# Kernel optimization log

Hardware: AMD Instinct MI355X
Metric: run time of the kernel (lower is better)

The kernel has to match this reference:

```python
import math
import jax, jax.numpy as jnp
import numpy as np

NUM_OPS = 7
NUM_STAGES = 2
TAU = 1.0


def _stage(x, labels_f, logits_k, mag_neg_k, mag_pos_k, key):
    # One augmentation stage: gumbel-softmax weighted mix of 7 ops, fully vectorized over batch.
    B, C, T = x.shape
    dt = x.dtype
    ks = jax.random.split(key, 7)
    # Gumbel-softmax (soft) over op logits
    g = -jnp.log(-jnp.log(jax.random.uniform(ks[0], (NUM_OPS,), minval=1e-20, maxval=1.0)))
    w = jax.nn.softmax((logits_k + g.astype(logits_k.dtype)) / TAU)
    # per-sample, per-op magnitudes: |mag_neg + label*(mag_pos - mag_neg)|  -> (B, NUM_OPS)
    mag = jnp.abs(mag_neg_k[None, :] + labels_f[:, None] * (mag_pos_k - mag_neg_k)[None, :])
    t_idx = jnp.arange(T)
    t2pi = jnp.linspace(0.0, 2.0 * math.pi, T).astype(dt)
    # op0: gaussian noise
    y0 = x + mag[:, 0, None, None] * jax.random.normal(ks[1], x.shape, dt)
    # op1: magnitude scale
    y1 = x * (1.0 + mag[:, 1, None, None])
    # op2: time mask (zero contiguous segment of length floor(mag*T), random start per sample)
    ml = jnp.clip(jnp.floor(mag[:, 2] * T).astype(jnp.int32), 0, T)
    u = jax.random.uniform(ks[2], (B,))
    start = jnp.floor(u * jnp.maximum(T - ml + 1, 1).astype(u.dtype)).astype(jnp.int32)
    masked = (t_idx[None, :] >= start[:, None]) & (t_idx[None, :] < (start + ml)[:, None])
    y2 = jnp.where(masked[:, None, :], jnp.zeros((), dt), x)
    # op3: baseline wander (low-frequency sinusoid)
    freq = jax.random.uniform(ks[3], (B,)) * 0.3 + 0.05
    ph = jax.random.uniform(ks[4], (B,)) * (2.0 * math.pi)
    wander = jnp.sin(freq[:, None].astype(dt) * t2pi[None, :] + ph[:, None].astype(dt))  # (B,T)
    y3 = x + mag[:, 3, None, None] * wander[:, None, :]
    # op4: temporal warp == grid_sample(bilinear, border padding, align_corners=True) on 1D time axis
    base = jnp.linspace(-1.0, 1.0, T).astype(dt)[None, :]
    wf = jax.random.uniform(ks[5], (B,)) * 2.0 + 1.0
    wp = jax.random.uniform(ks[6], (B,)) * (2.0 * math.pi)
    disp = 0.1 * mag[:, 4, None] * jnp.sin(wf[:, None].astype(dt) * t2pi[None, :] + wp[:, None].astype(dt))
    px = (jnp.clip(base + disp, -1.0, 1.0) + 1.0) * 0.5 * (T - 1)  # pixel coords in [0, T-1]
    i0 = jnp.clip(jnp.floor(px).astype(jnp.int32), 0, T - 1)
    i1 = jnp.clip(i0 + 1, 0, T - 1)
    frac = (px - i0.astype(dt))[:, None, :]
    xl = jnp.take_along_axis(x, jnp.broadcast_to(i0[:, None, :], x.shape), axis=2)
    xr = jnp.take_along_axis(x, jnp.broadcast_to(i1[:, None, :], x.shape), axis=2)
    y4 = xl * (1.0 - frac) + xr * frac
    # op5: temporal displacement (circular shift by floor(mag*T)); roll(s)[t] = x[(t - s) mod T]
    shift = jnp.floor(mag[:, 5] * T).astype(jnp.int32)
    ridx = jnp.mod(t_idx[None, :] - shift[:, None], T)
    y5 = jnp.take_along_axis(x, jnp.broadcast_to(ridx[:, None, :], x.shape), axis=2)
    # op6: no-op is x itself; weighted mix
    return (w[0] * y0 + w[1] * y1 + w[2] * y2 + w[3] * y3 + w[4] * y4 + w[5] * y5 + w[6] * x)


def setup_inputs() -> dict:
    key = jax.random.key(0)
    k1, k2, k3, k4, k5 = jax.random.split(key, 5)
    B, C, T = 128, 12, 5000
    x = jax.random.normal(k1, (B, C, T), jnp.float32)
    labels = jax.random.randint(k2, (B,), 0, 2)
    logits = jax.random.normal(k3, (NUM_STAGES, NUM_OPS), jnp.float32) * 0.1
    mag_neg = jax.random.uniform(k4, (NUM_STAGES, NUM_OPS), jnp.float32) * 0.2
    mag_pos = jax.random.uniform(k5, (NUM_STAGES, NUM_OPS), jnp.float32) * 0.2
    return {"x": x, "logits": logits, "mag_neg": mag_neg, "mag_pos": mag_pos, "labels": labels}


def reference(x, logits, mag_neg, mag_pos, labels):
    labels_f = labels.astype(x.dtype)
    base_key = jax.random.key(42)
    for k in range(NUM_STAGES):  # small fixed loop over stages (K=2)
        x = _stage(x, labels_f, logits[k], mag_neg[k], mag_pos[k], jax.random.fold_in(base_key, k))
    return x
```

## Files before the change

kernel.cpp:

```cpp
#include <hip/hip_runtime.h>
#include <stdint.h>

#pragma clang fp contract(off)

#define NB 128
#define NC 12
#define NTT 5000
#define BLK 320

typedef unsigned int u32;

__device__ __forceinline__ void tf2(u32 k0, u32 k1, u32 c0, u32 c1, u32& o0, u32& o1) {
  u32 k2 = k0 ^ k1 ^ 0x1BD11BDAu;
  u32 x0 = c0 + k0, x1 = c1 + k1;
#define TFR(r) x0 += x1; x1 = (x1 << (r)) | (x1 >> (32 - (r))); x1 ^= x0;
  TFR(13) TFR(15) TFR(26) TFR(6)
  x0 += k1; x1 += k2 + 1u;
  TFR(17) TFR(29) TFR(16) TFR(24)
  x0 += k2; x1 += k0 + 2u;
  TFR(13) TFR(15) TFR(26) TFR(6)
  x0 += k0; x1 += k1 + 3u;
  TFR(17) TFR(29) TFR(16) TFR(24)
  x0 += k1; x1 += k2 + 4u;
  TFR(13) TFR(15) TFR(26) TFR(6)
  x0 += k2; x1 += k0 + 5u;
#undef TFR
  o0 = x0; o1 = x1;
}

__device__ __forceinline__ float u01(u32 bits) {
  return __uint_as_float((bits >> 9) | 0x3F800000u) - 1.0f;
}

__device__ __forceinline__ float erfinv_poly(float xx) {
  float l = __builtin_amdgcn_logf(1.0f - xx);
  float p;
  if (l > -7.2134752f) {
    float w = fmaf(l, -0.69314718f, -2.5f);
    p = fmaf(2.81022636e-08f, w, 3.43273939e-07f);
    p = fmaf(p, w, -3.5233877e-06f);
    p = fmaf(p, w, -4.39150654e-06f);
    p = fmaf(p, w, 0.00021858087f);
    p = fmaf(p, w, -0.00125372503f);
    p = fmaf(p, w, -0.00417768164f);
    p = fmaf(p, w, 0.246640727f);
    p = fmaf(p, w, 1.50140941f);
  } else {
    float w = l * -0.69314718f;
    w = __fsqrt_rn(w) - 3.0f;
    p = fmaf(-0.000200214257f, w, 0.000100950558f);
    p = fmaf(p, w, 0.00134934322f);
    p = fmaf(p, w, -0.00367342844f);
    p = fmaf(p, w, 0.00573950773f);
    p = fmaf(p, w, -0.0076224613f);
    p = fmaf(p, w, 0.00943887047f);
    p = fmaf(p, w, 1.00167406f);
    p = fmaf(p, w, 2.83297682f);
  }
  return p;
}

struct SSc {
  float w[7];
  float mag0, scale1, mag3, amp4, freq, ph, wf, wp;
  int start, mlen, shift;
  u32 nk0, nk1;
};

__global__ __launch_bounds__(BLK, 8) void aug_fused(
    const float* __restrict__ xin, const float* __restrict__ logits,
    const float* __restrict__ mag_neg, const float* __restrict__ mag_pos,
    const int* __restrict__ labels, float* __restrict__ xout) {
  __shared__ float rowB[NTT + 1];
  __shared__ SSc ssc[2];

  const int bc = blockIdx.x;
  const int b = bc / NC;
  const int rowbase = bc * NTT;
  const int tid = threadIdx.x;

  if (tid < 64) {
    bool nz = labels[2 * tid + 1] != 0;
    unsigned long long mk = __ballot(nz);
    const int mode64 = (mk == 0ULL) ? 1 : 0;
    const int L = tid;
    if (L < 14) {
      const int s = (L >= 7) ? 1 : 0;
      const int j = L - 7 * s;
      const int lab = mode64 ? labels[2 * b] : labels[b];
      const float lf = (float)lab;

      u32 kk0, kk1, kj0, kj1, k00, k01, o0, o1;
      tf2(0u, 42u, 0u, (u32)s, kk0, kk1);
      tf2(kk0, kk1, 0u, (u32)j, kj0, kj1);
      tf2(kk0, kk1, 0u, 0u, k00, k01);
      tf2(k00, k01, 0u, (u32)j, o0, o1);
      float u = fmaxf(u01(o0 ^ o1), 1e-20f);
      float g = -__logf(-__logf(u));
      float v = logits[s * 7 + j] + g;

      float vk[7];
#pragma unroll
      for (int k = 0; k < 7; ++k) vk[k] = __shfl(v, 7 * s + k);
      float m = vk[0];
#pragma unroll
      for (int k = 1; k < 7; ++k) m = fmaxf(m, vk[k]);
      float sum = 0.0f;
#pragma unroll
      for (int k = 0; k < 7; ++k) sum += __expf(vk[k] - m);
      ssc[s].w[j] = __expf(v - m) / sum;

      float mn = mag_neg[s * 7 + j];
      float mp = mag_pos[s * 7 + j];
      float d = mp - mn;
      float pr = lf * d;
      float mgj = fabsf(mn + pr);

      if (j == 0) {
        ssc[s].mag0 = mgj;
      } else if (j == 1) {
        ssc[s].scale1 = 1.0f + mgj;
        ssc[s].nk0 = kj0; ssc[s].nk1 = kj1;
      } else if (j == 2) {
        int ml = (int)floorf(mgj * 5000.0f);
        ml = ml < 0 ? 0 : (ml > NTT ? NTT : ml);
        tf2(kj0, kj1, 0u, (u32)b, o0, o1);
        int tml = NTT - ml + 1;
        if (tml < 1) tml = 1;
        int st = (int)floorf(u01(o0 ^ o1) * (float)tml);
        ssc[s].start = st; ssc[s].mlen = ml;
      } else if (j == 3) {
        ssc[s].mag3 = mgj;
        tf2(kj0, kj1, 0u, (u32)b, o0, o1);
        float f = u01(o0 ^ o1); float fp = f * 0.3f; ssc[s].freq = fp + 0.05f;
      } else if (j == 4) {
        ssc[s].amp4 = 0.1f * mgj;
        tf2(kj0, kj1, 0u, (u32)b, o0, o1);
        ssc[s].ph = u01(o0 ^ o1) * 6.283185307179586f;
      } else if (j == 5) {
        ssc[s].shift = (int)floorf(mgj * 5000.0f);
        tf2(kj0, kj1, 0u, (u32)b, o0, o1);
        float f = u01(o0 ^ o1); float fp = f * 2.0f; ssc[s].wf = fp + 1.0f;
      } else {
        tf2(kj0, kj1, 0u, (u32)b, o0, o1);
        ssc[s].wp = u01(o0 ^ o1) * 6.283185307179586f;
      }
    }
  }
  __syncthreads();

  const float D_T2PI = 6.283185307179586f / 4999.0f;
  const float D_BASE = 2.0f / 4999.0f;
  const float NLO = -0.9999999403953552f;
  const float SQRT2 = 1.4142135623730951f;

  {
    const SSc sc = ssc[0];
    const float cc_m = ((sc.w[0] + sc.w[1] * sc.scale1) + sc.w[3]) + sc.w[6];
    const float cc_u = cc_m + sc.w[2];
    const float A0s = (sc.w[0] * sc.mag0) * SQRT2;
    const float A3 = sc.w[3] * sc.mag3;
    const float W4 = sc.w[4], W5 = sc.w[5];
    const float fD3 = sc.freq * D_T2PI;
    const float fD4 = sc.wf * D_T2PI;
    const u32 mstart = (u32)sc.start, mlen = (u32)sc.mlen;
    const u32 nk0 = sc.nk0, nk1 = sc.nk1;
    const float* __restrict__ rx = xin + rowbase;

    if (tid == 0) rowB[NTT] = 0.0f;

#pragma unroll 4
    for (int t = tid; t < NTT; t += BLK) {
      float tf = (float)t;
      float sin3 = __sinf(fmaf(tf, fD3, sc.ph));
      float sin4 = __sinf(fmaf(tf, fD4, sc.wp));

      float posb = fmaf(tf, D_BASE, -1.0f);
      float p = fmaf(sc.amp4, sin4, posb);
      p = fminf(1.0f, fmaxf(-1.0f, p));
      float px = fmaf(p, 2499.5f, 2499.5f);
      int i0 = (int)px;
      int i1 = min(i0 + 1, NTT - 1);
      float fr = px - (float)i0;

      int rt = t - sc.shift;
      if (rt < 0) rt += NTT;

      float xv = rx[t];
      float xl = rx[i0];
      float xr = rx[i1];
      float xs = rx[rt];

      u32 o0, o1;
      tf2(nk0, nk1, 0u, (u32)(rowbase + t), o0, o1);
      float f = u01(o0 ^ o1);
      float un = fmaf(f, 2.0f, NLO);
      float ei = erfinv_poly(un * un) * un;

      float cc = ((u32)(t - (int)mstart) < mlen) ? cc_m : cc_u;

      float y4 = fmaf(xr - xl, fr, xl);
      float r = xv * cc;
      r = fmaf(A0s, ei, r);
      r = fmaf(A3, sin3, r);
      r = fmaf(W4, y4, r);
      r = fmaf(W5, xs, r);

      rowB[t] = r;
    }
  }
  __syncthreads();

  {
    const SSc sc = ssc[1];
    const float cc_m = ((sc.w[0] + sc.w[1] * sc.scale1) + sc.w[3]) + sc.w[6];
    const float cc_u = cc_m + sc.w[2];
    const float A0s = (sc.w[0] * sc.mag0) * SQRT2;
    const float A3 = sc.w[3] * sc.mag3;
    const float W4 = sc.w[4], W5 = sc.w[5];
    const float fD3 = sc.freq * D_T2PI;
    const float fD4 = sc.wf * D_T2PI;
    const u32 mstart = (u32)sc.start, mlen = (u32)sc.mlen;
    const u32 nk0 = sc.nk0, nk1 = sc.nk1;

#pragma unroll 4
    for (int t = tid; t < NTT; t += BLK) {
      float tf = (float)t;
      float sin3 = __sinf(fmaf(tf, fD3, sc.ph));
      float sin4 = __sinf(fmaf(tf, fD4, sc.wp));

      float posb = fmaf(tf, D_BASE, -1.0f);
      float p = fmaf(sc.amp4, sin4, posb);
      p = fminf(1.0f, fmaxf(-1.0f, p));
      float px = fmaf(p, 2499.5f, 2499.5f);
      int i0 = (int)px;
      float fr = px - (float)i0;

      int rt = t - sc.shift;
      if (rt < 0) rt += NTT;

      float xv = rowB[t];
      float xl = rowB[i0];
      float xr = rowB[i0 + 1];
      float xs = rowB[rt];

      u32 o0, o1;
      tf2(nk0, nk1, 0u, (u32)(rowbase + t), o0, o1);
      float f = u01(o0 ^ o1);
      float un = fmaf(f, 2.0f, NLO);
      float ei = erfinv_poly(un * un) * un;

      float cc = ((u32)(t - (int)mstart) < mlen) ? cc_m : cc_u;

      float y4 = fmaf(xr - xl, fr, xl);
      float r = xv * cc;
      r = fmaf(A0s, ei, r);
      r = fmaf(A3, sin3, r);
      r = fmaf(W4, y4, r);
      r = fmaf(W5, xs, r);

      xout[rowbase + t] = r;
    }
  }
}

extern "C" void kernel_launch(void* const* d_in, const int* in_sizes, int n_in,
                              void* d_out, int out_size, void* d_ws, size_t ws_size,
                              hipStream_t stream) {
  (void)in_sizes; (void)n_in; (void)d_ws; (void)ws_size; (void)out_size;
  const float* x = (const float*)d_in[0];
  const float* logits = (const float*)d_in[1];
  const float* mag_neg = (const float*)d_in[2];
  const float* mag_pos = (const float*)d_in[3];
  const int* labels = (const int*)d_in[4];
  float* out = (float*)d_out;
  hipLaunchKernelGGL(aug_fused, dim3(NB * NC), dim3(BLK), 0, stream,
                     x, logits, mag_neg, mag_pos, labels, out);
}
```

Baseline: 71.29 us.

## Split fused two-stage kernel into two balanced flat-partitioned stage kernels

```diff
diff --git a/kernel.cpp b/kernel.cpp
--- a/kernel.cpp
+++ b/kernel.cpp
@@ -3,10 +3,14 @@
 
 #pragma clang fp contract(off)
 
-#define NB 128
-#define NC 12
+#define NBATCH 128
+#define NCH 12
 #define NTT 5000
-#define BLK 320
+#define NROWS (NBATCH * NCH)
+#define TOTAL (NROWS * NTT)
+#define BLK 256
+#define NBLK 2048
+#define BELEM (TOTAL / NBLK)
 
 typedef unsigned int u32;
 
@@ -67,7 +71,168 @@
   u32 nk0, nk1;
 };
 
-__global__ __launch_bounds__(BLK, 8) void aug_fused(
+__device__ __forceinline__ void derive_op(SSc* dst, int stage, int j, int b,
+    int mode64, const float* __restrict__ logits,
+    const float* __restrict__ mag_neg, const float* __restrict__ mag_pos,
+    const int* __restrict__ labels, int lanebase) {
+  const int lab = mode64 ? labels[2 * b] : labels[b];
+  const float lf = (float)lab;
+
+  u32 kk0, kk1, kj0, kj1, k00, k01, o0, o1;
+  tf2(0u, 42u, 0u, (u32)stage, kk0, kk1);
+  tf2(kk0, kk1, 0u, (u32)j, kj0, kj1);
+  tf2(kk0, kk1, 0u, 0u, k00, k01);
+  tf2(k00, k01, 0u, (u32)j, o0, o1);
+  float u = fmaxf(u01(o0 ^ o1), 1e-20f);
+  float g = -__logf(-__logf(u));
+  float v = logits[stage * 7 + j] + g;
+
+  float vk[7];
+#pragma unroll
+  for (int k = 0; k < 7; ++k) vk[k] = __shfl(v, lanebase + k);
+  float m = vk[0];
+#pragma unroll
+  for (int k = 1; k < 7; ++k) m = fmaxf(m, vk[k]);
+  float sum = 0.0f;
+#pragma unroll
+  for (int k = 0; k < 7; ++k) sum += __expf(vk[k] - m);
+  dst->w[j] = __expf(v - m) / sum;
+
+  float mn = mag_neg[stage * 7 + j];
+  float mp = mag_pos[stage * 7 + j];
+  float d = mp - mn;
+  float pr = lf * d;
+  float mgj = fabsf(mn + pr);
+
+  if (j == 0) {
+    dst->mag0 = mgj;
+  } else if (j == 1) {
+    dst->scale1 = 1.0f + mgj;
+    dst->nk0 = kj0; dst->nk1 = kj1;
+  } else if (j == 2) {
+    int ml = (int)floorf(mgj * 5000.0f);
+    ml = ml < 0 ? 0 : (ml > NTT ? NTT : ml);
+    tf2(kj0, kj1, 0u, (u32)b, o0, o1);
+    int tml = NTT - ml + 1;
+    if (tml < 1) tml = 1;
+    int st = (int)floorf(u01(o0 ^ o1) * (float)tml);
+    dst->start = st; dst->mlen = ml;
+  } else if (j == 3) {
+    dst->mag3 = mgj;
+    tf2(kj0, kj1, 0u, (u32)b, o0, o1);
+    float f = u01(o0 ^ o1); float fp = f * 0.3f; dst->freq = fp + 0.05f;
+  } else if (j == 4) {
+    dst->amp4 = 0.1f * mgj;
+    tf2(kj0, kj1, 0u, (u32)b, o0, o1);
+    dst->ph = u01(o0 ^ o1) * 6.283185307179586f;
+  } else if (j == 5) {
+    dst->shift = (int)floorf(mgj * 5000.0f);
+    tf2(kj0, kj1, 0u, (u32)b, o0, o1);
+    float f = u01(o0 ^ o1); float fp = f * 2.0f; dst->wf = fp + 1.0f;
+  } else {
+    tf2(kj0, kj1, 0u, (u32)b, o0, o1);
+    dst->wp = u01(o0 ^ o1) * 6.283185307179586f;
+  }
+}
+
+template <int STRIDE>
+__device__ __forceinline__ void run_seg(const SSc& sc, int ts, int te, int rowbase,
+    const float* __restrict__ sr, float* __restrict__ dr, int tid) {
+  const float NLO = -0.9999999403953552f;
+  const float SQRT2 = 1.4142135623730951f;
+  const float D_T2PI = 6.283185307179586f / 4999.0f;
+  const float D_BASE = 2.0f / 4999.0f;
+
+  const float cc_m = ((sc.w[0] + sc.w[1] * sc.scale1) + sc.w[3]) + sc.w[6];
+  const float cc_u = cc_m + sc.w[2];
+  const float A0s = (sc.w[0] * sc.mag0) * SQRT2;
+  const float A3 = sc.w[3] * sc.mag3;
+  const float W4 = sc.w[4], W5 = sc.w[5];
+  const float fD3 = sc.freq * D_T2PI;
+  const float fD4 = sc.wf * D_T2PI;
+  const u32 mstart = (u32)sc.start, mlen = (u32)sc.mlen;
+  const u32 nk0 = sc.nk0, nk1 = sc.nk1;
+
+#pragma unroll 4
+  for (int t = ts + tid; t < te; t += STRIDE) {
+    float tf = (float)t;
+    float sin3 = __sinf(fmaf(tf, fD3, sc.ph));
+    float sin4 = __sinf(fmaf(tf, fD4, sc.wp));
+
+    float posb = fmaf(tf, D_BASE, -1.0f);
+    float p = fmaf(sc.amp4, sin4, posb);
+    p = fminf(1.0f, fmaxf(-1.0f, p));
+    float px = fmaf(p, 2499.5f, 2499.5f);
+    int i0 = (int)px;
+    int i1 = min(i0 + 1, NTT - 1);
+    float fr = px - (float)i0;
+
+    int rt = t - sc.shift;
+    if (rt < 0) rt += NTT;
+
+    float xv = sr[t];
+    float xl = sr[i0];
+    float xr = sr[i1];
+    float xs = sr[rt];
+
+    u32 o0, o1;
+    tf2(nk0, nk1, 0u, (u32)(rowbase + t), o0, o1);
+    float f = u01(o0 ^ o1);
+    float un = fmaf(f, 2.0f, NLO);
+    float ei = erfinv_poly(un * un) * un;
+
+    float cc = ((u32)(t - (int)mstart) < mlen) ? cc_m : cc_u;
+
+    float y4 = fmaf(xr - xl, fr, xl);
+    float r = xv * cc;
+    r = fmaf(A0s, ei, r);
+    r = fmaf(A3, sin3, r);
+    r = fmaf(W4, y4, r);
+    r = fmaf(W5, xs, r);
+
+    dr[t] = r;
+  }
+}
+
+__global__ __launch_bounds__(BLK, 8) void aug_stage(
+    const float* __restrict__ src, float* __restrict__ dst,
+    const float* __restrict__ logits, const float* __restrict__ mag_neg,
+    const float* __restrict__ mag_pos, const int* __restrict__ labels,
+    int stage) {
+  __shared__ SSc ssc[2];
+  const int bid = blockIdx.x;
+  const int tid = threadIdx.x;
+  const int e0 = bid * BELEM, e1 = e0 + BELEM;
+  const int r0 = e0 / NTT;
+  const int rlast = (e1 - 1) / NTT;
+  const int nrows = rlast - r0 + 1;
+
+  if (tid < 64) {
+    bool nz = labels[2 * tid + 1] != 0;
+    unsigned long long mk = __ballot(nz);
+    const int mode64 = (mk == 0ULL) ? 1 : 0;
+    const int slot = tid >> 3;
+    const int j = tid & 7;
+    if (tid < 16 && j < 7 && slot < nrows) {
+      const int row = slot ? rlast : r0;
+      derive_op(&ssc[slot], stage, j, row / NCH, mode64,
+                logits, mag_neg, mag_pos, labels, slot * 8);
+    }
+  }
+  __syncthreads();
+
+  const int mid = min(e1, (r0 + 1) * NTT);
+  {
+    const int rb = r0 * NTT;
+    run_seg<BLK>(ssc[0], e0 - rb, mid - rb, rb, src + rb, dst + rb, tid);
+  }
+  if (nrows == 2) {
+    const int rb = rlast * NTT;
+    run_seg<BLK>(ssc[1], 0, e1 - rb, rb, src + rb, dst + rb, tid);
+  }
+}
+
+__global__ __launch_bounds__(256, 6) void aug_fused(
     const float* __restrict__ xin, const float* __restrict__ logits,
     const float* __restrict__ mag_neg, const float* __restrict__ mag_pos,
     const int* __restrict__ labels, float* __restrict__ xout) {
@@ -75,7 +240,7 @@
   __shared__ SSc ssc[2];
 
   const int bc = blockIdx.x;
-  const int b = bc / NC;
+  const int b = bc / NCH;
   const int rowbase = bc * NTT;
   const int tid = threadIdx.x;
 
@@ -83,79 +248,24 @@
     bool nz = labels[2 * tid + 1] != 0;
     unsigned long long mk = __ballot(nz);
     const int mode64 = (mk == 0ULL) ? 1 : 0;
-    const int L = tid;
-    if (L < 14) {
-      const int s = (L >= 7) ? 1 : 0;
-      const int j = L - 7 * s;
-      const int lab = mode64 ? labels[2 * b] : labels[b];
-      const float lf = (float)lab;
-
-      u32 kk0, kk1, kj0, kj1, k00, k01, o0, o1;
-      tf2(0u, 42u, 0u, (u32)s, kk0, kk1);
-      tf2(kk0, kk1, 0u, (u32)j, kj0, kj1);
-      tf2(kk0, kk1, 0u, 0u, k00, k01);
-      tf2(k00, k01, 0u, (u32)j, o0, o1);
-      float u = fmaxf(u01(o0 ^ o1), 1e-20f);
-      float g = -__logf(-__logf(u));
-      float v = logits[s * 7 + j] + g;
-
-      float vk[7];
-#pragma unroll
-      for (int k = 0; k < 7; ++k) vk[k] = __shfl(v, 7 * s + k);
-      float m = vk[0];
-#pragma unroll
-      for (int k = 1; k < 7; ++k) m = fmaxf(m, vk[k]);
-      float sum = 0.0f;
-#pragma unroll
-      for (int k = 0; k < 7; ++k) sum += __expf(vk[k] - m);
-      ssc[s].w[j] = __expf(v - m) / sum;
-
-      float mn = mag_neg[s * 7 + j];
-      float mp = mag_pos[s * 7 + j];
-      float d = mp - mn;
-      float pr = lf * d;
-      float mgj = fabsf(mn + pr);
-
-      if (j == 0) {
-        ssc[s].mag0 = mgj;
-      } else if (j == 1) {
-        ssc[s].scale1 = 1.0f + mgj;
-        ssc[s].nk0 = kj0; ssc[s].nk1 = kj1;
-      } else if (j == 2) {
-        int ml = (int)floorf(mgj * 5000.0f);
-        ml = ml < 0 ? 0 : (ml > NTT ? NTT : ml);
-        tf2(kj0, kj1, 0u, (u32)b, o0, o1);
-        int tml = NTT - ml + 1;
-        if (tml < 1) tml = 1;
-        int st = (int)floorf(u01(o0 ^ o1) * (float)tml);
-        ssc[s].start = st; ssc[s].mlen = ml;
-      } else if (j == 3) {
-        ssc[s].mag3 = mgj;
-        tf2(kj0, kj1, 0u, (u32)b, o0, o1);
-        float f = u01(o0 ^ o1); float fp = f * 0.3f; ssc[s].freq = fp + 0.05f;
-      } else if (j == 4) {
-        ssc[s].amp4 = 0.1f * mgj;
-        tf2(kj0, kj1, 0u, (u32)b, o0, o1);
-        ssc[s].ph = u01(o0 ^ o1) * 6.283185307179586f;
-      } else if (j == 5) {
-        ssc[s].shift = (int)floorf(mgj * 5000.0f);
-        tf2(kj0, kj1, 0u, (u32)b, o0, o1);
-        float f = u01(o0 ^ o1); float fp = f * 2.0f; ssc[s].wf = fp + 1.0f;
-      } else {
-        tf2(kj0, kj1, 0u, (u32)b, o0, o1);
-        ssc[s].wp = u01(o0 ^ o1) * 6.283185307179586f;
-      }
+    if (tid < 14) {
+      const int s = (tid >= 7) ? 1 : 0;
+      const int j = tid - 7 * s;
+      derive_op(&ssc[s], s, j, b, mode64,
+                logits, mag_neg, mag_pos, labels, 7 * s);
     }
   }
+  if (tid == 0) rowB[NTT] = 0.0f;
   __syncthreads();
 
-  const float D_T2PI = 6.283185307179586f / 4999.0f;
-  const float D_BASE = 2.0f / 4999.0f;
-  const float NLO = -0.9999999403953552f;
-  const float SQRT2 = 1.4142135623730951f;
+  run_seg<256>(ssc[0], 0, NTT, rowbase, xin + rowbase, rowB, tid);
+  __syncthreads();
 
   {
-    const SSc sc = ssc[0];
+    const SSc sc = ssc[1];
+    const float NLO = -0.9999999403953552f, SQRT2 = 1.4142135623730951f;
+    const float D_T2PI = 6.283185307179586f / 4999.0f;
+    const float D_BASE = 2.0f / 4999.0f;
     const float cc_m = ((sc.w[0] + sc.w[1] * sc.scale1) + sc.w[3]) + sc.w[6];
     const float cc_u = cc_m + sc.w[2];
     const float A0s = (sc.w[0] * sc.mag0) * SQRT2;
@@ -164,101 +274,29 @@
     const float fD3 = sc.freq * D_T2PI;
     const float fD4 = sc.wf * D_T2PI;
     const u32 mstart = (u32)sc.start, mlen = (u32)sc.mlen;
-    const u32 nk0 = sc.nk0, nk1 = sc.nk1;
-    const float* __restrict__ rx = xin + rowbase;
-
-    if (tid == 0) rowB[NTT] = 0.0f;
-
 #pragma unroll 4
-    for (int t = tid; t < NTT; t += BLK) {
+    for (int t = tid; t < NTT; t += 256) {
       float tf = (float)t;
       float sin3 = __sinf(fmaf(tf, fD3, sc.ph));
       float sin4 = __sinf(fmaf(tf, fD4, sc.wp));
-
-      float posb = fmaf(tf, D_BASE, -1.0f);
-      float p = fmaf(sc.amp4, sin4, posb);
-      p = fminf(1.0f, fmaxf(-1.0f, p));
-      float px = fmaf(p, 2499.5f, 2499.5f);
-      int i0 = (int)px;
-      int i1 = min(i0 + 1, NTT - 1);
-      float fr = px - (float)i0;
-
-      int rt = t - sc.shift;
-      if (rt < 0) rt += NTT;
-
-      float xv = rx[t];
-      float xl = rx[i0];
-      float xr = rx[i1];
-      float xs = rx[rt];
-
-      u32 o0, o1;
-      tf2(nk0, nk1, 0u, (u32)(rowbase + t), o0, o1);
-      float f = u01(o0 ^ o1);
-      float un = fmaf(f, 2.0f, NLO);
-      float ei = erfinv_poly(un * un) * un;
-
-      float cc = ((u32)(t - (int)mstart) < mlen) ? cc_m : cc_u;
-
-      float y4 = fmaf(xr - xl, fr, xl);
-      float r = xv * cc;
-      r = fmaf(A0s, ei, r);
-      r = fmaf(A3, sin3, r);
-      r = fmaf(W4, y4, r);
-      r = fmaf(W5, xs, r);
-
-      rowB[t] = r;
-    }
-  }
-  __syncthreads();
-
-  {
-    const SSc sc = ssc[1];
-    const float cc_m = ((sc.w[0] + sc.w[1] * sc.scale1) + sc.w[3]) + sc.w[6];
-    const float cc_u = cc_m + sc.w[2];
-    const float A0s = (sc.w[0] * sc.mag0) * SQRT2;
-    const float A3 = sc.w[3] * sc.mag3;
-    const float W4 = sc.w[4], W5 = sc.w[5];
-    const float fD3 = sc.freq * D_T2PI;
-    const float fD4 = sc.wf * D_T2PI;
-    const u32 mstart = (u32)sc.start, mlen = (u32)sc.mlen;
-    const u32 nk0 = sc.nk0, nk1 = sc.nk1;
-
-#pragma unroll 4
-    for (int t = tid; t < NTT; t += BLK) {
-      float tf = (float)t;
-      float sin3 = __sinf(fmaf(tf, fD3, sc.ph));
-      float sin4 = __sinf(fmaf(tf, fD4, sc.wp));
-
       float posb = fmaf(tf, D_BASE, -1.0f);
       float p = fmaf(sc.amp4, sin4, posb);
       p = fminf(1.0f, fmaxf(-1.0f, p));
       float px = fmaf(p, 2499.5f, 2499.5f);
       int i0 = (int)px;
       float fr = px - (float)i0;
-
       int rt = t - sc.shift;
       if (rt < 0) rt += NTT;
-
-      float xv = rowB[t];
-      float xl = rowB[i0];
-      float xr = rowB[i0 + 1];
-      float xs = rowB[rt];
-
-      u32 o0, o1;
-      tf2(nk0, nk1, 0u, (u32)(rowbase + t), o0, o1);
+      float xv = rowB[t], xl = rowB[i0], xr = rowB[i0 + 1], xs = rowB[rt];
+      u32 o0, o1; tf2(sc.nk0, sc.nk1, 0u, (u32)(rowbase + t), o0, o1);
       float f = u01(o0 ^ o1);
       float un = fmaf(f, 2.0f, NLO);
       float ei = erfinv_poly(un * un) * un;
-
       float cc = ((u32)(t - (int)mstart) < mlen) ? cc_m : cc_u;
-
       float y4 = fmaf(xr - xl, fr, xl);
       float r = xv * cc;
-      r = fmaf(A0s, ei, r);
-      r = fmaf(A3, sin3, r);
-      r = fmaf(W4, y4, r);
-      r = fmaf(W5, xs, r);
-
+      r = fmaf(A0s, ei, r); r = fmaf(A3, sin3, r);
+      r = fmaf(W4, y4, r); r = fmaf(W5, xs, r);
       xout[rowbase + t] = r;
     }
   }
@@ -267,13 +305,22 @@
 extern "C" void kernel_launch(void* const* d_in, const int* in_sizes, int n_in,
                               void* d_out, int out_size, void* d_ws, size_t ws_size,
                               hipStream_t stream) {
-  (void)in_sizes; (void)n_in; (void)d_ws; (void)ws_size; (void)out_size;
+  (void)in_sizes; (void)n_in; (void)out_size;
   const float* x = (const float*)d_in[0];
   const float* logits = (const float*)d_in[1];
   const float* mag_neg = (const float*)d_in[2];
   const float* mag_pos = (const float*)d_in[3];
   const int* labels = (const int*)d_in[4];
   float* out = (float*)d_out;
-  hipLaunchKernelGGL(aug_fused, dim3(NB * NC), dim3(BLK), 0, stream,
-                     x, logits, mag_neg, mag_pos, labels, out);
-}
+
+  if (ws_size >= (size_t)TOTAL * sizeof(float) && d_ws != nullptr) {
+    float* y = (float*)d_ws;
+    hipLaunchKernelGGL(aug_stage, dim3(NBLK), dim3(BLK), 0, stream,
+                       x, y, logits, mag_neg, mag_pos, labels, 0);
+    hipLaunchKernelGGL(aug_stage, dim3(NBLK), dim3(BLK), 0, stream,
+                       y, out, logits, mag_neg, mag_pos, labels, 1);
+  } else {
+    hipLaunchKernelGGL(aug_fused, dim3(NROWS), dim3(256), 0, stream,
+                       x, logits, mag_neg, mag_pos, labels, out);
+  }
+}
```

New measurement: 71.02 us. About the same (-0.4%).
